# Performance work log

Measured on AMD Instinct MI355X. Metric: run time of the kernel, lower is better.

The kernel has to match this reference:

```python
import jax, jax.numpy as jnp
import numpy as np

B, S, DIM = 32, 1, 4096
N_HEADS, N_KV, HD = 32, 8, 128
N_REP = N_HEADS // N_KV
MAX_SEQ = 2048


def _rope(x, cos, sin):
    # x: [b, s, h, d]; cos/sin: [s, d//2]; rotate consecutive pairs
    x2 = x.reshape(*x.shape[:-1], HD // 2, 2)
    x0, x1 = x2[..., 0], x2[..., 1]
    c = cos[None, :, None, :]
    s = sin[None, :, None, :]
    o0 = x0 * c - x1 * s
    o1 = x0 * s + x1 * c
    return jnp.stack([o0, o1], axis=-1).reshape(x.shape)


def setup_inputs() -> dict:
    key = jax.random.key(0)
    ks = jax.random.split(key, 9)
    start_pos = 2047
    # true RoPE frequencies at position start_pos
    inv_freq = 1.0 / (10000.0 ** (np.arange(0, HD, 2, dtype=np.float32) / HD))
    ang = (start_pos * inv_freq).astype(np.float32)[None, :]  # [1, HD//2]
    return {
        "x": jax.random.normal(ks[0], (B, S, DIM), jnp.float32),
        "freqs_cos": jnp.asarray(np.cos(ang)),
        "freqs_sin": jnp.asarray(np.sin(ang)),
        "wq": jax.random.normal(ks[1], (DIM, DIM), jnp.float32) * 0.02,
        "wk": jax.random.normal(ks[2], (N_KV * HD, DIM), jnp.float32) * 0.02,
        "wv": jax.random.normal(ks[3], (N_KV * HD, DIM), jnp.float32) * 0.02,
        "wo": jax.random.normal(ks[4], (DIM, DIM), jnp.float32) * 0.02,
        "cache_k": jax.random.normal(ks[5], (B, MAX_SEQ, N_KV, HD), jnp.float32),
        "cache_v": jax.random.normal(ks[6], (B, MAX_SEQ, N_KV, HD), jnp.float32),
        "start_pos": start_pos,
    }


def reference(x, freqs_cos, freqs_sin, wq, wk, wv, wo, cache_k, cache_v, start_pos):
    b, s, dim = x.shape  # s == 1 (decode)
    xq = (x @ wq.T).reshape(b, s, N_HEADS, HD)
    xk = (x @ wk.T).reshape(b, s, N_KV, HD)
    xv = (x @ wv.T).reshape(b, s, N_KV, HD)
    xq = _rope(xq, freqs_cos, freqs_sin)
    xk = _rope(xk, freqs_cos, freqs_sin)
    # KV-cache scatter write at start_pos
    cache_k = jax.lax.dynamic_update_slice(cache_k, xk, (0, start_pos, 0, 0))
    cache_v = jax.lax.dynamic_update_slice(cache_v, xv, (0, start_pos, 0, 0))
    t = start_pos + s
    keys = cache_k[:, :t]    # [b, t, kv, hd]
    values = cache_v[:, :t]  # [b, t, kv, hd]
    # GQA: group query heads over kv heads (no repeat_kv materialization)
    q = xq[:, 0].reshape(b, N_KV, N_REP, HD)  # [b, kv, rep, hd]
    scale = HD ** -0.5
    attn = jnp.einsum("bkrd,btkd->bkrt", q, keys) * scale  # [b, kv, rep, t]
    attn = jax.nn.softmax(attn.astype(jnp.float32), axis=-1).astype(q.dtype)
    out = jnp.einsum("bkrt,btkd->bkrd", attn, values).reshape(b, s, dim)
    return out @ wo.T
```

## Files before the change

### kernel.cpp

```cpp
#include <hip/hip_runtime.h>
#include <math.h>

#define B_ 32
#define DIM_ 4096
#define NKV_ 8
#define HD_ 128
#define T_ 2048
#define KS_ 16
#define QKV_ROWS_ 6144
#define O_ROWS_ 4096
#define NSPLIT_ 4

#define Q_OFF    0
#define KNEW_OFF (Q_OFF + B_*DIM_)
#define VNEW_OFF (KNEW_OFF + B_*NKV_*HD_)
#define AO_OFF   (VNEW_OFF + B_*NKV_*HD_)
#define PQKV_OFF (AO_OFF + B_*DIM_)
#define PO_OFF   (PQKV_OFF + KS_*QKV_ROWS_*B_)
#define OPART_OFF (PO_OFF + KS_*O_ROWS_*B_)
#define ML_OFF   (OPART_OFF + B_*NKV_*NSPLIT_*4*HD_)

__device__ __forceinline__ void fma4(float4& a, const float4& x, float w) {
    a.x = fmaf(x.x, w, a.x); a.y = fmaf(x.y, w, a.y);
    a.z = fmaf(x.z, w, a.z); a.w = fmaf(x.w, w, a.w);
}

template<int NROWS>
__global__ __launch_bounds__(256) void gemm_split(
    const float* __restrict__ X, const float* __restrict__ W0,
    const float* __restrict__ W1, const float* __restrict__ W2,
    float* __restrict__ part)
{
    __shared__ float xs[32][36];
    __shared__ float wsh[32][132];
    const int rb = blockIdx.x, ks = blockIdx.y;
    const int row0 = rb * 128;
    const float* W; int wr0;
    if (NROWS == 4096 || row0 < 4096) { W = W0; wr0 = row0; }
    else if (row0 < 5120)             { W = W1; wr0 = row0 - 4096; }
    else                              { W = W2; wr0 = row0 - 5120; }
    const int tid = threadIdx.x;
    const int rt = tid & 31, bt = tid >> 5;
    float4 acc[4];
    acc[0] = acc[1] = acc[2] = acc[3] = make_float4(0.f,0.f,0.f,0.f);
    const int kc0 = ks * 256;
    const int xb = tid >> 3, xkq = tid & 7;
    for (int kt = 0; kt < 8; ++kt) {
        const int kc = kc0 + kt * 32;
        __syncthreads();
        {
            float4 v = *(const float4*)(X + xb * DIM_ + kc + xkq * 4);
            xs[xkq*4+0][xb] = v.x; xs[xkq*4+1][xb] = v.y;
            xs[xkq*4+2][xb] = v.z; xs[xkq*4+3][xb] = v.w;
        }
        #pragma unroll
        for (int j = 0; j < 4; ++j) {
            int f = tid + 256 * j;
            int r = f >> 3, kq = f & 7;
            float4 v = *(const float4*)(W + (wr0 + r) * DIM_ + kc + kq * 4);
            wsh[kq*4+0][r] = v.x; wsh[kq*4+1][r] = v.y;
            wsh[kq*4+2][r] = v.z; wsh[kq*4+3][r] = v.w;
        }
        __syncthreads();
        #pragma unroll
        for (int k = 0; k < 32; ++k) {
            float4 xv = *(const float4*)&xs[k][bt*4];
            float4 wv = *(const float4*)&wsh[k][rt*4];
            fma4(acc[0], xv, wv.x);
            fma4(acc[1], xv, wv.y);
            fma4(acc[2], xv, wv.z);
            fma4(acc[3], xv, wv.w);
        }
    }
    #pragma unroll
    for (int j = 0; j < 4; ++j) {
        const int row = row0 + rt * 4 + j;
        *(float4*)(part + (ks * NROWS + row) * 32 + bt * 4) = acc[j];
    }
}

__global__ __launch_bounds__(256) void reduce_rope(
    const float* __restrict__ part, const float* __restrict__ fc,
    const float* __restrict__ fs, float* __restrict__ qout,
    float* __restrict__ kout, float* __restrict__ vout)
{
    const int t = blockIdx.x * 256 + threadIdx.x;
    const int b = t & 31;
    const int row0 = (t >> 5) * 2;
    float s0 = 0.f, s1 = 0.f;
    #pragma unroll
    for (int ks = 0; ks < KS_; ++ks) {
        const float* p = part + (ks * QKV_ROWS_ + row0) * 32 + b;
        s0 += p[0];
        s1 += p[32];
    }
    if (row0 < 5120) {
        const int i = (row0 & 127) >> 1;
        const float c = fc[i], s = fs[i];
        const float o0 = s0 * c - s1 * s;
        const float o1 = s0 * s + s1 * c;
        if (row0 < 4096) {
            qout[b * 4096 + row0]     = o0;
            qout[b * 4096 + row0 + 1] = o1;
        } else {
            const int lr = row0 - 4096;
            kout[b * 1024 + lr]     = o0;
            kout[b * 1024 + lr + 1] = o1;
        }
    } else {
        const int lr = row0 - 5120;
        vout[b * 1024 + lr]     = s0;
        vout[b * 1024 + lr + 1] = s1;
    }
}

__global__ __launch_bounds__(256, 4) void attn_split(
    const float* __restrict__ q, const float* __restrict__ knew,
    const float* __restrict__ vnew, const float* __restrict__ ck,
    const float* __restrict__ cv, float* __restrict__ opart,
    float* __restrict__ ml)
{
    __shared__ float sct[512 * 4];
    __shared__ float red[2048];
    const int sp = blockIdx.x & 3;
    const int kv = (blockIdx.x >> 2) & 7;
    const int b  = blockIdx.x >> 5;
    const int tid = threadIdx.x;
    const int w  = tid >> 6;
    const int ln = tid & 63;
    const int t0 = sp * 512;
    const float scale = 0.08838834764831845f;

    const int tl = ln >> 4, dsl = ln & 15;
    float4 qr[4][2];
    #pragma unroll
    for (int r = 0; r < 4; ++r) {
        const float* qp = q + b * 4096 + (kv * 4 + r) * 128 + dsl * 8;
        qr[r][0] = *(const float4*)qp;
        qr[r][1] = *(const float4*)(qp + 4);
    }
    const float* ckb = ck + ((size_t)(b * 2048) * 8 + kv) * 128;
    const float* knb = knew + (b * 8 + kv) * 128 + dsl * 8;

    for (int tt = 0; tt < 32; tt += 4) {
        float4 ka[4][2];
        int ri[4];
        #pragma unroll
        for (int u = 0; u < 4; ++u) {
            ri[u] = w * 128 + (tt + u) * 4 + tl;
            const int gt = t0 + ri[u];
            const float* kp = (gt == 2047) ? knb
                              : (ckb + (size_t)gt * 1024 + dsl * 8);
            ka[u][0] = *(const float4*)kp;
            ka[u][1] = *(const float4*)(kp + 4);
        }
        #pragma unroll
        for (int u = 0; u < 4; ++u) {
            float d[4];
            #pragma unroll
            for (int r = 0; r < 4; ++r) {
                float t1 = ka[u][0].x*qr[r][0].x + ka[u][0].y*qr[r][0].y
                         + ka[u][0].z*qr[r][0].z + ka[u][0].w*qr[r][0].w;
                float t2 = ka[u][1].x*qr[r][1].x + ka[u][1].y*qr[r][1].y
                         + ka[u][1].z*qr[r][1].z + ka[u][1].w*qr[r][1].w;
                float dd = t1 + t2;
                dd += __shfl_xor(dd, 1);
                dd += __shfl_xor(dd, 2);
                dd += __shfl_xor(dd, 4);
                dd += __shfl_xor(dd, 8);
                d[r] = dd * scale;
            }
            if (dsl == 0)
                *(float4*)&sct[ri[u] * 4] = make_float4(d[0], d[1], d[2], d[3]);
        }
    }
    __syncthreads();

    float vals[8];
    #pragma unroll
    for (int j = 0; j < 8; ++j)
        vals[j] = sct[(j * 64 + ln) * 4 + w];
    float m = vals[0];
    #pragma unroll
    for (int j = 1; j < 8; ++j) m = fmaxf(m, vals[j]);
    #pragma unroll
    for (int o = 1; o < 64; o <<= 1)
        m = fmaxf(m, __shfl_xor(m, o));
    float l = 0.f;
    #pragma unroll
    for (int j = 0; j < 8; ++j) {
        const float p = __expf(vals[j] - m);
        sct[(j * 64 + ln) * 4 + w] = p;
        l += p;
    }
    #pragma unroll
    for (int o = 1; o < 64; o <<= 1)
        l += __shfl_xor(l, o);
    if (ln == 0) {
        const int idx = ((b * 8 + kv) * 4 + sp) * 8 + w * 2;
        ml[idx]     = m;
        ml[idx + 1] = l;
    }
    __syncthreads();

    float2 acc[4];
    #pragma unroll
    for (int r = 0; r < 4; ++r) acc[r] = make_float2(0.f, 0.f);
    const float* cvb = cv + ((size_t)(b * 2048) * 8 + kv) * 128 + ln * 2;
    const float* vnb = vnew + (b * 8 + kv) * 128 + ln * 2;
    for (int j = 0; j < 128; j += 8) {
        float2 vv[8];
        #pragma unroll
        for (int u = 0; u < 8; ++u) {
            const int gt = t0 + w * 128 + j + u;
            const float* vp = (gt == 2047) ? vnb : (cvb + (size_t)gt * 1024);
            vv[u] = *(const float2*)vp;
        }
        #pragma unroll
        for (int u = 0; u < 8; ++u) {
            const int ri = w * 128 + j + u;
            const float4 p4 = *(const float4*)&sct[ri * 4];
            acc[0].x = fmaf(vv[u].x, p4.x, acc[0].x);
            acc[0].y = fmaf(vv[u].y, p4.x, acc[0].y);
            acc[1].x = fmaf(vv[u].x, p4.y, acc[1].x);
            acc[1].y = fmaf(vv[u].y, p4.y, acc[1].y);
            acc[2].x = fmaf(vv[u].x, p4.z, acc[2].x);
            acc[2].y = fmaf(vv[u].y, p4.z, acc[2].y);
            acc[3].x = fmaf(vv[u].x, p4.w, acc[3].x);
            acc[3].y = fmaf(vv[u].y, p4.w, acc[3].y);
        }
    }
    #pragma unroll
    for (int r = 0; r < 4; ++r)
        *(float2*)&red[((w * 4 + r) * 64 + ln) * 2] = acc[r];
    __syncthreads();
    {
        const int r = tid >> 6, dd = tid & 63;
        float2 s = make_float2(0.f, 0.f);
        #pragma unroll
        for (int ww = 0; ww < 4; ++ww) {
            const float2 v = *(const float2*)&red[((ww * 4 + r) * 64 + dd) * 2];
            s.x += v.x; s.y += v.y;
        }
        const int ob = (((b * 8 + kv) * 4 + sp) * 4 + r) * 128 + dd * 2;
        *(float2*)&opart[ob] = s;
    }
}

__global__ __launch_bounds__(128) void attn_merge(
    const float* __restrict__ opart, const float* __restrict__ ml,
    float* __restrict__ ao)
{
    const int bk = blockIdx.x;
    const int tid = threadIdx.x;
    const int r = tid >> 5, dq = tid & 31;
    float m[4], l[4];
    #pragma unroll
    for (int sp = 0; sp < 4; ++sp) {
        m[sp] = ml[(bk * 4 + sp) * 8 + r * 2];
        l[sp] = ml[(bk * 4 + sp) * 8 + r * 2 + 1];
    }
    const float M = fmaxf(fmaxf(m[0], m[1]), fmaxf(m[2], m[3]));
    float wgt[4], L = 0.f;
    #pragma unroll
    for (int sp = 0; sp < 4; ++sp) {
        wgt[sp] = __expf(m[sp] - M);
        L += l[sp] * wgt[sp];
    }
    float4 o = make_float4(0.f, 0.f, 0.f, 0.f);
    #pragma unroll
    for (int sp = 0; sp < 4; ++sp) {
        const float4 v = *(const float4*)&opart[((bk * 4 + sp) * 4 + r) * 128 + dq * 4];
        fma4(o, v, wgt[sp]);
    }
    const float inv = 1.f / L;
    o.x *= inv; o.y *= inv; o.z *= inv; o.w *= inv;
    *(float4*)&ao[bk * 512 + r * 128 + dq * 4] = o;
}

__global__ __launch_bounds__(256) void reduce_out(
    const float* __restrict__ part, float* __restrict__ out)
{
    const int t = blockIdx.x * 256 + threadIdx.x;
    const int b = t & 31, row = t >> 5;
    float s = 0.f;
    #pragma unroll
    for (int ks = 0; ks < KS_; ++ks)
        s += part[(ks * O_ROWS_ + row) * 32 + b];
    out[b * 4096 + row] = s;
}

extern "C" void kernel_launch(void* const* d_in, const int* in_sizes, int n_in,
                              void* d_out, int out_size, void* d_ws, size_t ws_size,
                              hipStream_t stream)
{
    const float* x  = (const float*)d_in[0];
    const float* fc = (const float*)d_in[1];
    const float* fs = (const float*)d_in[2];
    const float* wq = (const float*)d_in[3];
    const float* wk = (const float*)d_in[4];
    const float* wv = (const float*)d_in[5];
    const float* wo = (const float*)d_in[6];
    const float* ck = (const float*)d_in[7];
    const float* cv = (const float*)d_in[8];
    float* ws    = (float*)d_ws;
    float* q     = ws + Q_OFF;
    float* knew  = ws + KNEW_OFF;
    float* vnew  = ws + VNEW_OFF;
    float* ao    = ws + AO_OFF;
    float* pqkv  = ws + PQKV_OFF;
    float* po    = ws + PO_OFF;
    float* opart = ws + OPART_OFF;
    float* mlp   = ws + ML_OFF;

    gemm_split<QKV_ROWS_><<<dim3(48, 16), 256, 0, stream>>>(x, wq, wk, wv, pqkv);
    reduce_rope<<<384, 256, 0, stream>>>(pqkv, fc, fs, q, knew, vnew);
    attn_split<<<1024, 256, 0, stream>>>(q, knew, vnew, ck, cv, opart, mlp);
    attn_merge<<<256, 128, 0, stream>>>(opart, mlp, ao);
    gemm_split<O_ROWS_><<<dim3(32, 16), 256, 0, stream>>>(ao, wo, wo, wo, po);
    reduce_out<<<512, 256, 0, stream>>>(po, (float*)d_out);
}
```

Measured before the change: 648.2 us.

## Restructure decode attention so each wave covers all KV heads, prefetch GEMM tiles

Attention is reorganised so each block handles one batch and a 128-token chunk. Each wave processes 32 tokens across all 8 KV heads, so every cache row is read as a full contiguous 4KB line, and there are 64 softmax splits per head instead of 4. The merge kernel now combines 64 partials, which adds workspace traffic and makes it heavier. Separately, the split GEMM now loads the next K-tile into registers while computing the current one, at the cost of more register pressure.

```diff
diff --git a/kernel.cpp b/kernel.cpp
--- a/kernel.cpp
+++ b/kernel.cpp
@@ -9,7 +9,8 @@
 #define KS_ 16
 #define QKV_ROWS_ 6144
 #define O_ROWS_ 4096
-#define NSPLIT_ 4
+#define NCHUNK_ 16
+#define NSPLITW_ 64
 
 #define Q_OFF    0
 #define KNEW_OFF (Q_OFF + B_*DIM_)
@@ -18,7 +19,7 @@
 #define PQKV_OFF (AO_OFF + B_*DIM_)
 #define PO_OFF   (PQKV_OFF + KS_*QKV_ROWS_*B_)
 #define OPART_OFF (PO_OFF + KS_*O_ROWS_*B_)
-#define ML_OFF   (OPART_OFF + B_*NKV_*NSPLIT_*4*HD_)
+#define ML_OFF   (OPART_OFF + B_*NKV_*NSPLITW_*4*HD_)
 
 __device__ __forceinline__ void fma4(float4& a, const float4& x, float w) {
     a.x = fmaf(x.x, w, a.x); a.y = fmaf(x.y, w, a.y);
@@ -45,23 +46,29 @@
     acc[0] = acc[1] = acc[2] = acc[3] = make_float4(0.f,0.f,0.f,0.f);
     const int kc0 = ks * 256;
     const int xb = tid >> 3, xkq = tid & 7;
+    float4 xpf, wpf[4];
+    xpf = *(const float4*)(X + xb * DIM_ + kc0 + xkq * 4);
+    #pragma unroll
+    for (int j = 0; j < 4; ++j)
+        wpf[j] = *(const float4*)(W + (wr0 + xb + 32*j) * DIM_ + kc0 + xkq * 4);
     for (int kt = 0; kt < 8; ++kt) {
-        const int kc = kc0 + kt * 32;
         __syncthreads();
-        {
-            float4 v = *(const float4*)(X + xb * DIM_ + kc + xkq * 4);
-            xs[xkq*4+0][xb] = v.x; xs[xkq*4+1][xb] = v.y;
-            xs[xkq*4+2][xb] = v.z; xs[xkq*4+3][xb] = v.w;
-        }
+        xs[xkq*4+0][xb] = xpf.x; xs[xkq*4+1][xb] = xpf.y;
+        xs[xkq*4+2][xb] = xpf.z; xs[xkq*4+3][xb] = xpf.w;
         #pragma unroll
         for (int j = 0; j < 4; ++j) {
-            int f = tid + 256 * j;
-            int r = f >> 3, kq = f & 7;
-            float4 v = *(const float4*)(W + (wr0 + r) * DIM_ + kc + kq * 4);
-            wsh[kq*4+0][r] = v.x; wsh[kq*4+1][r] = v.y;
-            wsh[kq*4+2][r] = v.z; wsh[kq*4+3][r] = v.w;
+            const int r = xb + 32*j;
+            wsh[xkq*4+0][r] = wpf[j].x; wsh[xkq*4+1][r] = wpf[j].y;
+            wsh[xkq*4+2][r] = wpf[j].z; wsh[xkq*4+3][r] = wpf[j].w;
         }
         __syncthreads();
+        if (kt < 7) {
+            const int kc = kc0 + (kt + 1) * 32;
+            xpf = *(const float4*)(X + xb * DIM_ + kc + xkq * 4);
+            #pragma unroll
+            for (int j = 0; j < 4; ++j)
+                wpf[j] = *(const float4*)(W + (wr0 + xb + 32*j) * DIM_ + kc + xkq * 4);
+        }
         #pragma unroll
         for (int k = 0; k < 32; ++k) {
             float4 xv = *(const float4*)&xs[k][bt*4];
@@ -114,137 +121,119 @@
     }
 }
 
-__global__ __launch_bounds__(256, 4) void attn_split(
+__global__ __launch_bounds__(256, 2) void attn_split(
     const float* __restrict__ q, const float* __restrict__ knew,
     const float* __restrict__ vnew, const float* __restrict__ ck,
     const float* __restrict__ cv, float* __restrict__ opart,
     float* __restrict__ ml)
 {
-    __shared__ float sct[512 * 4];
-    __shared__ float red[2048];
-    const int sp = blockIdx.x & 3;
-    const int kv = (blockIdx.x >> 2) & 7;
-    const int b  = blockIdx.x >> 5;
+    __shared__ float sct[4][32 * 33];
+    const int chunk = blockIdx.x & 15;
+    const int b     = blockIdx.x >> 4;
     const int tid = threadIdx.x;
-    const int w  = tid >> 6;
-    const int ln = tid & 63;
-    const int t0 = sp * 512;
+    const int w  = tid >> 6, ln = tid & 63;
+    const int kvl = ln >> 3, dsl = ln & 7;
+    const int t0 = chunk * 128 + w * 32;
+    const int split = chunk * 4 + w;
     const float scale = 0.08838834764831845f;
-
-    const int tl = ln >> 4, dsl = ln & 15;
-    float4 qr[4][2];
+    float* ss = sct[w];
+
+    float4 qr[4][4];
     #pragma unroll
     for (int r = 0; r < 4; ++r) {
-        const float* qp = q + b * 4096 + (kv * 4 + r) * 128 + dsl * 8;
-        qr[r][0] = *(const float4*)qp;
-        qr[r][1] = *(const float4*)(qp + 4);
-    }
-    const float* ckb = ck + ((size_t)(b * 2048) * 8 + kv) * 128;
-    const float* knb = knew + (b * 8 + kv) * 128 + dsl * 8;
-
-    for (int tt = 0; tt < 32; tt += 4) {
-        float4 ka[4][2];
-        int ri[4];
-        #pragma unroll
-        for (int u = 0; u < 4; ++u) {
-            ri[u] = w * 128 + (tt + u) * 4 + tl;
-            const int gt = t0 + ri[u];
-            const float* kp = (gt == 2047) ? knb
-                              : (ckb + (size_t)gt * 1024 + dsl * 8);
-            ka[u][0] = *(const float4*)kp;
-            ka[u][1] = *(const float4*)(kp + 4);
-        }
-        #pragma unroll
-        for (int u = 0; u < 4; ++u) {
+        const float* qp = q + b * 4096 + (kvl * 4 + r) * 128 + dsl * 16;
+        #pragma unroll
+        for (int j = 0; j < 4; ++j) qr[r][j] = *(const float4*)(qp + j * 4);
+    }
+    const float* ckb = ck + (size_t)b * (2048 * 1024) + kvl * 128 + dsl * 16;
+    const float* knb = knew + (b * 8 + kvl) * 128 + dsl * 16;
+
+    for (int tt = 0; tt < 32; tt += 2) {
+        float4 ka[2][4];
+        #pragma unroll
+        for (int u = 0; u < 2; ++u) {
+            const int gt = t0 + tt + u;
+            const float* kp = (gt == 2047) ? knb : (ckb + (size_t)gt * 1024);
+            #pragma unroll
+            for (int j = 0; j < 4; ++j) ka[u][j] = *(const float4*)(kp + j * 4);
+        }
+        #pragma unroll
+        for (int u = 0; u < 2; ++u) {
             float d[4];
             #pragma unroll
             for (int r = 0; r < 4; ++r) {
-                float t1 = ka[u][0].x*qr[r][0].x + ka[u][0].y*qr[r][0].y
-                         + ka[u][0].z*qr[r][0].z + ka[u][0].w*qr[r][0].w;
-                float t2 = ka[u][1].x*qr[r][1].x + ka[u][1].y*qr[r][1].y
-                         + ka[u][1].z*qr[r][1].z + ka[u][1].w*qr[r][1].w;
-                float dd = t1 + t2;
-                dd += __shfl_xor(dd, 1);
-                dd += __shfl_xor(dd, 2);
-                dd += __shfl_xor(dd, 4);
-                dd += __shfl_xor(dd, 8);
-                d[r] = dd * scale;
+                float s = 0.f;
+                #pragma unroll
+                for (int j = 0; j < 4; ++j) {
+                    s = fmaf(ka[u][j].x, qr[r][j].x, s);
+                    s = fmaf(ka[u][j].y, qr[r][j].y, s);
+                    s = fmaf(ka[u][j].z, qr[r][j].z, s);
+                    s = fmaf(ka[u][j].w, qr[r][j].w, s);
+                }
+                s += __shfl_xor(s, 1);
+                s += __shfl_xor(s, 2);
+                s += __shfl_xor(s, 4);
+                d[r] = s * scale;
             }
-            if (dsl == 0)
-                *(float4*)&sct[ri[u] * 4] = make_float4(d[0], d[1], d[2], d[3]);
+            float out = d[0];
+            const int dr = dsl & 3;
+            if (dr == 1) out = d[1];
+            if (dr == 2) out = d[2];
+            if (dr == 3) out = d[3];
+            if (dsl < 4) ss[(kvl * 4 + dsl) * 33 + tt + u] = out;
         }
     }
     __syncthreads();
 
-    float vals[8];
-    #pragma unroll
-    for (int j = 0; j < 8; ++j)
-        vals[j] = sct[(j * 64 + ln) * 4 + w];
-    float m = vals[0];
-    #pragma unroll
-    for (int j = 1; j < 8; ++j) m = fmaxf(m, vals[j]);
-    #pragma unroll
-    for (int o = 1; o < 64; o <<= 1)
-        m = fmaxf(m, __shfl_xor(m, o));
-    float l = 0.f;
-    #pragma unroll
-    for (int j = 0; j < 8; ++j) {
-        const float p = __expf(vals[j] - m);
-        sct[(j * 64 + ln) * 4 + w] = p;
-        l += p;
-    }
-    #pragma unroll
-    for (int o = 1; o < 64; o <<= 1)
-        l += __shfl_xor(l, o);
-    if (ln == 0) {
-        const int idx = ((b * 8 + kv) * 4 + sp) * 8 + w * 2;
-        ml[idx]     = m;
-        ml[idx + 1] = l;
+    if (ln < 32) {
+        float mx = -1e30f;
+        #pragma unroll
+        for (int t = 0; t < 32; ++t) mx = fmaxf(mx, ss[ln * 33 + t]);
+        float sum = 0.f;
+        #pragma unroll
+        for (int t = 0; t < 32; ++t) {
+            const float p = __expf(ss[ln * 33 + t] - mx);
+            ss[ln * 33 + t] = p;
+            sum += p;
+        }
+        const int kvp = ln >> 2, rp = ln & 3;
+        *(float2*)(ml + (size_t)(((b * 8 + kvp) * 64 + split) * 4 + rp) * 2)
+            = make_float2(mx, sum);
     }
     __syncthreads();
 
-    float2 acc[4];
-    #pragma unroll
-    for (int r = 0; r < 4; ++r) acc[r] = make_float2(0.f, 0.f);
-    const float* cvb = cv + ((size_t)(b * 2048) * 8 + kv) * 128 + ln * 2;
-    const float* vnb = vnew + (b * 8 + kv) * 128 + ln * 2;
-    for (int j = 0; j < 128; j += 8) {
-        float2 vv[8];
-        #pragma unroll
-        for (int u = 0; u < 8; ++u) {
-            const int gt = t0 + w * 128 + j + u;
+    float4 acc[4][4];
+    #pragma unroll
+    for (int r = 0; r < 4; ++r)
+        #pragma unroll
+        for (int j = 0; j < 4; ++j) acc[r][j] = make_float4(0.f,0.f,0.f,0.f);
+    const float* cvb = cv + (size_t)b * (2048 * 1024) + kvl * 128 + dsl * 16;
+    const float* vnb = vnew + (b * 8 + kvl) * 128 + dsl * 16;
+    for (int tt = 0; tt < 32; tt += 2) {
+        float4 va[2][4];
+        #pragma unroll
+        for (int u = 0; u < 2; ++u) {
+            const int gt = t0 + tt + u;
             const float* vp = (gt == 2047) ? vnb : (cvb + (size_t)gt * 1024);
-            vv[u] = *(const float2*)vp;
-        }
-        #pragma unroll
-        for (int u = 0; u < 8; ++u) {
-            const int ri = w * 128 + j + u;
-            const float4 p4 = *(const float4*)&sct[ri * 4];
-            acc[0].x = fmaf(vv[u].x, p4.x, acc[0].x);
-            acc[0].y = fmaf(vv[u].y, p4.x, acc[0].y);
-            acc[1].x = fmaf(vv[u].x, p4.y, acc[1].x);
-            acc[1].y = fmaf(vv[u].y, p4.y, acc[1].y);
-            acc[2].x = fmaf(vv[u].x, p4.z, acc[2].x);
-            acc[2].y = fmaf(vv[u].y, p4.z, acc[2].y);
-            acc[3].x = fmaf(vv[u].x, p4.w, acc[3].x);
-            acc[3].y = fmaf(vv[u].y, p4.w, acc[3].y);
-        }
-    }
+            #pragma unroll
+            for (int j = 0; j < 4; ++j) va[u][j] = *(const float4*)(vp + j * 4);
+        }
+        #pragma unroll
+        for (int u = 0; u < 2; ++u) {
+            #pragma unroll
+            for (int r = 0; r < 4; ++r) {
+                const float p = ss[(kvl * 4 + r) * 33 + tt + u];
+                #pragma unroll
+                for (int j = 0; j < 4; ++j) fma4(acc[r][j], va[u][j], p);
+            }
+        }
+    }
+    float* ob = opart + (size_t)(((b * 8 + kvl) * 64 + split) * 4) * 128 + dsl * 16;
     #pragma unroll
     for (int r = 0; r < 4; ++r)
-        *(float2*)&red[((w * 4 + r) * 64 + ln) * 2] = acc[r];
-    __syncthreads();
-    {
-        const int r = tid >> 6, dd = tid & 63;
-        float2 s = make_float2(0.f, 0.f);
-        #pragma unroll
-        for (int ww = 0; ww < 4; ++ww) {
-            const float2 v = *(const float2*)&red[((ww * 4 + r) * 64 + dd) * 2];
-            s.x += v.x; s.y += v.y;
-        }
-        const int ob = (((b * 8 + kv) * 4 + sp) * 4 + r) * 128 + dd * 2;
-        *(float2*)&opart[ob] = s;
-    }
+        #pragma unroll
+        for (int j = 0; j < 4; ++j)
+            *(float4*)(ob + r * 128 + j * 4) = acc[r][j];
 }
 
 __global__ __launch_bounds__(128) void attn_merge(
@@ -254,28 +243,24 @@
     const int bk = blockIdx.x;
     const int tid = threadIdx.x;
     const int r = tid >> 5, dq = tid & 31;
-    float m[4], l[4];
-    #pragma unroll
-    for (int sp = 0; sp < 4; ++sp) {
-        m[sp] = ml[(bk * 4 + sp) * 8 + r * 2];
-        l[sp] = ml[(bk * 4 + sp) * 8 + r * 2 + 1];
-    }
-    const float M = fmaxf(fmaxf(m[0], m[1]), fmaxf(m[2], m[3]));
-    float wgt[4], L = 0.f;
-    #pragma unroll
-    for (int sp = 0; sp < 4; ++sp) {
-        wgt[sp] = __expf(m[sp] - M);
-        L += l[sp] * wgt[sp];
-    }
+    float M = -1e30f;
+    #pragma unroll 8
+    for (int sp = 0; sp < NSPLITW_; ++sp)
+        M = fmaxf(M, ml[(size_t)((bk * 64 + sp) * 4 + r) * 2]);
+    float L = 0.f;
     float4 o = make_float4(0.f, 0.f, 0.f, 0.f);
-    #pragma unroll
-    for (int sp = 0; sp < 4; ++sp) {
-        const float4 v = *(const float4*)&opart[((bk * 4 + sp) * 4 + r) * 128 + dq * 4];
-        fma4(o, v, wgt[sp]);
+    #pragma unroll 4
+    for (int sp = 0; sp < NSPLITW_; ++sp) {
+        const float2 mlv = *(const float2*)(ml + (size_t)((bk * 64 + sp) * 4 + r) * 2);
+        const float wgt = __expf(mlv.x - M);
+        L += mlv.y * wgt;
+        const float4 v = *(const float4*)(opart
+            + (size_t)((bk * 64 + sp) * 4 + r) * 128 + dq * 4);
+        fma4(o, v, wgt);
     }
     const float inv = 1.f / L;
     o.x *= inv; o.y *= inv; o.z *= inv; o.w *= inv;
-    *(float4*)&ao[bk * 512 + r * 128 + dq * 4] = o;
+    *(float4*)(ao + bk * 512 + r * 128 + dq * 4) = o;
 }
 
 __global__ __launch_bounds__(256) void reduce_out(
@@ -315,7 +300,7 @@
 
     gemm_split<QKV_ROWS_><<<dim3(48, 16), 256, 0, stream>>>(x, wq, wk, wv, pqkv);
     reduce_rope<<<384, 256, 0, stream>>>(pqkv, fc, fs, q, knew, vnew);
-    attn_split<<<1024, 256, 0, stream>>>(q, knew, vnew, ck, cv, opart, mlp);
+    attn_split<<<512, 256, 0, stream>>>(q, knew, vnew, ck, cv, opart, mlp);
     attn_merge<<<256, 128, 0, stream>>>(opart, mlp, ao);
     gemm_split<O_ROWS_><<<dim3(32, 16), 256, 0, stream>>>(ao, wo, wo, wo, po);
     reduce_out<<<512, 256, 0, stream>>>(po, (float*)d_out);
```

After: 670.2 us. 3.4% more time.
